# Kernel tuning notes

Measured on AMD Instinct MI355X. Metric: run time of the kernel, lower is better.

The kernel has to match this reference:

```python
import jax, jax.numpy as jnp
from jax import lax
import numpy as np

E, D, I, T, K = 32, 1024, 512, 4096, 8

def setup_inputs() -> dict:
    key = jax.random.key(0)
    k1, k2, k3, k4, k5 = jax.random.split(key, 5)
    hidden_states = jax.random.normal(k1, (T, D), dtype=jnp.float32)
    top_k_indices = jax.random.randint(k2, (T, K), 0, E, dtype=jnp.int64)
    w = jax.random.uniform(k3, (T, K), dtype=jnp.float32)
    top_k_weights = w / jnp.sum(w, axis=-1, keepdims=True)  # normalised routing weights
    gate_up_proj = jax.random.normal(k4, (E, 2 * I, D), dtype=jnp.float32) * 0.05
    down_proj = jax.random.normal(k5, (E, D, I), dtype=jnp.float32) * 0.05
    return {
        'hidden_states': hidden_states,
        'top_k_indices': top_k_indices,
        'top_k_weights': top_k_weights,
        'gate_up_proj': gate_up_proj,
        'down_proj': down_proj,
    }


def _moe(hidden_states, top_k_indices, top_k_weights, gate_up_proj, down_proj):
    num_experts = gate_up_proj.shape[0]
    # combine[t, e] = sum over k-slots routed to expert e of top_k_weights[t, k].
    # Duplicate expert ids in a token's top-k sum their weights, matching the
    # torch loop which index_add's each (k, tok) pair separately (outputs identical).
    onehot = jax.nn.one_hot(top_k_indices, num_experts, dtype=hidden_states.dtype)  # [T,K,E]
    combine = jnp.einsum('tke,tk->te', onehot, top_k_weights)  # [T,E]

    def body(acc, ew):
        W_gu, W_d, c = ew  # [2I,D], [D,I], [T]
        gu = hidden_states @ W_gu.T  # [T,2I]
        gate, up = jnp.split(gu, 2, axis=-1)
        h = jax.nn.silu(gate) * up  # SwiGLU
        y = h @ W_d.T  # [T,D]
        return acc + c[:, None] * y, None

    out, _ = lax.scan(body, jnp.zeros_like(hidden_states),
                      (gate_up_proj, down_proj, combine.T))
    return out


def reference(hidden_states, top_k_indices, top_k_weights, gate_up_proj, down_proj):
    return _moe(hidden_states, top_k_indices, top_k_weights, gate_up_proj, down_proj)
```

## Files before the change

kernel.cpp:

```cpp
#include <hip/hip_runtime.h>
#include <hip/hip_bf16.h>

#define E_   32
#define D_   1024
#define I_   512
#define T_   4096
#define KTOP 8
#define TK   (T_*KTOP)

#define BM   128
#define BKK  32
#define MAXT (TK/BM + E_)

#define TILES_OFF 1024
#define TOK_OFF   8192
#define WT_OFF    139264
#define H_OFF     524288

typedef __attribute__((ext_vector_type(8))) short short8v;
typedef __attribute__((ext_vector_type(4))) float f32x4;

__device__ inline unsigned short f2bf(float x) {
    union { float f; unsigned u; } v; v.f = x;
    return (unsigned short)((v.u + 0x7fff + ((v.u >> 16) & 1)) >> 16);
}
__device__ inline short8v pack8(float4 a, float4 b) {
    short8v r;
    r[0]=(short)f2bf(a.x); r[1]=(short)f2bf(a.y); r[2]=(short)f2bf(a.z); r[3]=(short)f2bf(a.w);
    r[4]=(short)f2bf(b.x); r[5]=(short)f2bf(b.y); r[6]=(short)f2bf(b.z); r[7]=(short)f2bf(b.w);
    return r;
}


__global__ void detect_idx64_kernel(const int* __restrict__ idx32, int* w) {
    if (threadIdx.x == 0 && blockIdx.x == 0) {
        int all0 = 1;
        for (int i = 0; i < 256; ++i)
            if (idx32[2*i + 1] != 0) { all0 = 0; break; }
        w[0] = all0;
    }
}

__global__ void count_kernel(const int* __restrict__ idx32, int* w) {
    int i = blockIdx.x * blockDim.x + threadIdx.x;
    if (i >= TK) return;
    int e = w[0] ? idx32[2*i] : idx32[i];
    atomicAdd(&w[32 + e], 1);
}

__global__ void scan_kernel(int* w) {
    if (threadIdx.x != 0 || blockIdx.x != 0) return;
    int off = 0;
    for (int e = 0; e < E_; ++e) { w[96 + e] = off; off += w[32 + e]; }
    w[96 + E_] = off;
    int2* tiles = (int2*)((char*)w + TILES_OFF);
    int nt = 0;
    for (int e = 0; e < E_; ++e)
        for (int rs = w[96 + e]; rs < w[96 + e + 1]; rs += BM)
            tiles[nt++] = make_int2(e, rs);
    w[129] = nt;
}

__global__ void scatter_kernel(const int* __restrict__ idx32,
                               const float* __restrict__ wts, int* w) {
    int i = blockIdx.x * blockDim.x + threadIdx.x;
    if (i >= TK) return;
    int e = w[0] ? idx32[2*i] : idx32[i];
    int p = atomicAdd(&w[64 + e], 1);
    int pos = w[96 + e] + p;
    ((int*)  ((char*)w + TOK_OFF))[pos] = i / KTOP;
    ((float*)((char*)w + WT_OFF))[pos]  = wts[i];
}

__global__ __launch_bounds__(256) void gemm1_mfma(
    const float* __restrict__ hidden, const float* __restrict__ gup,
    const int* __restrict__ w, unsigned short* __restrict__ H)
{
    if ((int)blockIdx.y >= w[129]) return;
    int2 tl = ((const int2*)((const char*)w + TILES_OFF))[blockIdx.y];
    const int e = tl.x, rs = tl.y;
    const int rows = min(w[96 + e + 1] - rs, BM);
    const int* tok = (const int*)((const char*)w + TOK_OFF);

    __shared__ short As[BM * BKK];
    __shared__ short Bs[BM * BKK];
    __shared__ int tokS[BM];

    const int tid = threadIdx.x;
    if (tid < BM) tokS[tid] = tok[rs + min(tid, rows - 1)];
    __syncthreads();

    const int n0 = blockIdx.x * 64;
    const float* gb = gup + (size_t)e * (2 * I_) * D_;

    const int crow = tid >> 2, ckg = tid & 3;
    const float* aptr0 = hidden + (size_t)tokS[crow]      * D_ + ckg * 8;
    const float* aptr1 = hidden + (size_t)tokS[crow + 64] * D_ + ckg * 8;
    const float* bptr0 = gb + (size_t)(n0 + crow)      * D_ + ckg * 8;
    const float* bptr1 = gb + (size_t)(I_ + n0 + crow) * D_ + ckg * 8;
    short8v* wA0 = (short8v*)&As[crow * BKK + ckg * 8];
    short8v* wA1 = (short8v*)&As[(crow + 64) * BKK + ckg * 8];
    short8v* wB0 = (short8v*)&Bs[crow * BKK + ckg * 8];
    short8v* wB1 = (short8v*)&Bs[(crow + 64) * BKK + ckg * 8];

    const int wid = tid >> 6, lane = tid & 63;
    const int l16 = lane & 15, lk = (lane >> 4) * 8;
    const int aoff = (wid * 32 + l16) * BKK + lk;
    const int boff = l16 * BKK + lk;

    f32x4 acc[2][8];
#pragma unroll
    for (int i = 0; i < 2; ++i)
#pragma unroll
        for (int j = 0; j < 8; ++j) acc[i][j] = (f32x4){0.f, 0.f, 0.f, 0.f};

    float4 ra0a, ra0b, ra1a, ra1b, rb0a, rb0b, rb1a, rb1b;
#define LOADREGS1(K0) { \
    ra0a = *(const float4*)(aptr0 + (K0)); ra0b = *(const float4*)(aptr0 + (K0) + 4); \
    ra1a = *(const float4*)(aptr1 + (K0)); ra1b = *(const float4*)(aptr1 + (K0) + 4); \
    rb0a = *(const float4*)(bptr0 + (K0)); rb0b = *(const float4*)(bptr0 + (K0) + 4); \
    rb1a = *(const float4*)(bptr1 + (K0)); rb1b = *(const float4*)(bptr1 + (K0) + 4); }

    LOADREGS1(0);
    for (int k0 = 0; k0 < D_; k0 += BKK) {
        __syncthreads();
        *wA0 = pack8(ra0a, ra0b);
        *wA1 = pack8(ra1a, ra1b);
        *wB0 = pack8(rb0a, rb0b);
        *wB1 = pack8(rb1a, rb1b);
        __syncthreads();
        if (k0 + BKK < D_) LOADREGS1(k0 + BKK);
        short8v a0 = *(const short8v*)&As[aoff];
        short8v a1 = *(const short8v*)&As[aoff + 16 * BKK];
#pragma unroll
        for (int j = 0; j < 8; ++j) {
            short8v b = *(const short8v*)&Bs[boff + j * 16 * BKK];
            acc[0][j] = __builtin_amdgcn_mfma_f32_16x16x32_bf16(a0, b, acc[0][j], 0, 0, 0);
            acc[1][j] = __builtin_amdgcn_mfma_f32_16x16x32_bf16(a1, b, acc[1][j], 0, 0, 0);
        }
    }

    const int r0 = (lane >> 4) * 4;
#pragma unroll
    for (int mr = 0; mr < 2; ++mr)
#pragma unroll
        for (int j = 0; j < 4; ++j)
#pragma unroll
            for (int r = 0; r < 4; ++r) {
                int m = wid * 32 + mr * 16 + r0 + r;
                if (m < rows) {
                    float g = acc[mr][j][r], u = acc[mr][j + 4][r];
                    float s = g / (1.f + __expf(-g));
                    H[(size_t)(rs + m) * I_ + n0 + j * 16 + l16] = f2bf(s * u);
                }
            }
}

__global__ __launch_bounds__(256) void gemm2_mfma(
    const unsigned short* __restrict__ H, const float* __restrict__ down,
    const int* __restrict__ w, float* __restrict__ out)
{
    if ((int)blockIdx.y >= w[129]) return;
    int2 tl = ((const int2*)((const char*)w + TILES_OFF))[blockIdx.y];
    const int e = tl.x, rs = tl.y;
    const int rows = min(w[96 + e + 1] - rs, BM);
    const int*   tok = (const int*)  ((const char*)w + TOK_OFF);
    const float* wts = (const float*)((const char*)w + WT_OFF);

    __shared__ short As[BM * BKK];
    __shared__ short Bs[BM * BKK];
    __shared__ int   tokS[BM];
    __shared__ float wtS[BM];

    const int tid = threadIdx.x;
    if (tid < BM) {
        tokS[tid] = tok[rs + min(tid, rows - 1)];
        wtS[tid]  = (tid < rows) ? wts[rs + tid] : 0.f;
    }
    __syncthreads();

    const int n0 = blockIdx.x * 128;
    const float* db = down + (size_t)e * D_ * I_;

    const int crow = tid >> 2, ckg = tid & 3;
    const short* ha0 = (const short*)H + (size_t)min(rs + crow,      TK - 1) * I_ + ckg * 8;
    const short* ha1 = (const short*)H + (size_t)min(rs + crow + 64, TK - 1) * I_ + ckg * 8;
    const float* bptr0 = db + (size_t)(n0 + crow)      * I_ + ckg * 8;
    const float* bptr1 = db + (size_t)(n0 + crow + 64) * I_ + ckg * 8;
    short8v* wA0 = (short8v*)&As[crow * BKK + ckg * 8];
    short8v* wA1 = (short8v*)&As[(crow + 64) * BKK + ckg * 8];
    short8v* wB0 = (short8v*)&Bs[crow * BKK + ckg * 8];
    short8v* wB1 = (short8v*)&Bs[(crow + 64) * BKK + ckg * 8];

    const int wid = tid >> 6, lane = tid & 63;
    const int l16 = lane & 15, lk = (lane >> 4) * 8;
    const int aoff = (wid * 32 + l16) * BKK + lk;
    const int boff = l16 * BKK + lk;

    f32x4 acc[2][8];
#pragma unroll
    for (int i = 0; i < 2; ++i)
#pragma unroll
        for (int j = 0; j < 8; ++j) acc[i][j] = (f32x4){0.f, 0.f, 0.f, 0.f};

    short8v raa, rab;
    float4 rb0a, rb0b, rb1a, rb1b;
#define LOADREGS2(K0) { \
    raa = *(const short8v*)(ha0 + (K0)); rab = *(const short8v*)(ha1 + (K0)); \
    rb0a = *(const float4*)(bptr0 + (K0)); rb0b = *(const float4*)(bptr0 + (K0) + 4); \
    rb1a = *(const float4*)(bptr1 + (K0)); rb1b = *(const float4*)(bptr1 + (K0) + 4); }

    LOADREGS2(0);
    for (int k0 = 0; k0 < I_; k0 += BKK) {
        __syncthreads();
        *wA0 = raa;
        *wA1 = rab;
        *wB0 = pack8(rb0a, rb0b);
        *wB1 = pack8(rb1a, rb1b);
        __syncthreads();
        if (k0 + BKK < I_) LOADREGS2(k0 + BKK);
        short8v a0 = *(const short8v*)&As[aoff];
        short8v a1 = *(const short8v*)&As[aoff + 16 * BKK];
#pragma unroll
        for (int j = 0; j < 8; ++j) {
            short8v b = *(const short8v*)&Bs[boff + j * 16 * BKK];
            acc[0][j] = __builtin_amdgcn_mfma_f32_16x16x32_bf16(a0, b, acc[0][j], 0, 0, 0);
            acc[1][j] = __builtin_amdgcn_mfma_f32_16x16x32_bf16(a1, b, acc[1][j], 0, 0, 0);
        }
    }

    const int r0 = (lane >> 4) * 4;
#pragma unroll
    for (int mr = 0; mr < 2; ++mr)
#pragma unroll
        for (int j = 0; j < 8; ++j)
#pragma unroll
            for (int r = 0; r < 4; ++r) {
                int m = wid * 32 + mr * 16 + r0 + r;
                if (m < rows)
                    atomicAdd(&out[(size_t)tokS[m] * D_ + n0 + j * 16 + l16],
                              wtS[m] * acc[mr][j][r]);
            }
}


extern "C" void kernel_launch(void* const* d_in, const int* in_sizes, int n_in,
                              void* d_out, int out_size, void* d_ws, size_t ws_size,
                              hipStream_t stream)
{
    const float* hidden = (const float*)d_in[0];
    const int*   idx    = (const int*)  d_in[1];
    const float* wts    = (const float*)d_in[2];
    const float* gup    = (const float*)d_in[3];
    const float* down   = (const float*)d_in[4];
    float* out = (float*)d_out;
    int*   w   = (int*)d_ws;

    hipMemsetAsync(d_ws, 0, 8192, stream);
    hipMemsetAsync(d_out, 0, (size_t)T_ * D_ * sizeof(float), stream);

    detect_idx64_kernel<<<1, 64, 0, stream>>>(idx, w);
    count_kernel<<<(TK + 255) / 256, 256, 0, stream>>>(idx, w);
    scan_kernel<<<1, 32, 0, stream>>>(w);
    scatter_kernel<<<(TK + 255) / 256, 256, 0, stream>>>(idx, wts, w);

    unsigned short* H = (unsigned short*)((char*)d_ws + H_OFF);
    dim3 g1(I_ / 64, MAXT), g2(D_ / 128, MAXT);
    gemm1_mfma<<<g1, 256, 0, stream>>>(hidden, gup, w, H);
    gemm2_mfma<<<g2, 256, 0, stream>>>(H, down, w, out);
}
```

Before: 733.0 us.

## Pad LDS tiles, parallelize scan and index detection, use library bf16 conversion

Pads the shared-memory A/B tiles from 32 to 40 shorts per row so the MFMA operand reads from LDS hit fewer bank conflicts. It also replaces the single-thread serial scan and tile-list construction with a wave-level shuffle prefix sum, and turns the int64-index detection loop into a parallel wave vote. The hand-written float-to-bf16 rounding is swapped for the HIP intrinsic. Together these target LDS conflict stalls in both GEMMs and serial latency in the small setup kernels, at the cost of more shared memory per block.

```diff
diff --git a/kernel.cpp b/kernel.cpp
--- a/kernel.cpp
+++ b/kernel.cpp
@@ -10,6 +10,7 @@
 
 #define BM   128
 #define BKK  32
+#define PAD  40
 #define MAXT (TK/BM + E_)
 
 #define TILES_OFF 1024
@@ -21,8 +22,8 @@
 typedef __attribute__((ext_vector_type(4))) float f32x4;
 
 __device__ inline unsigned short f2bf(float x) {
-    union { float f; unsigned u; } v; v.f = x;
-    return (unsigned short)((v.u + 0x7fff + ((v.u >> 16) & 1)) >> 16);
+    __hip_bfloat16 h = __float2bfloat16(x);
+    union { __hip_bfloat16 h; unsigned short u; } c; c.h = h; return c.u;
 }
 __device__ inline short8v pack8(float4 a, float4 b) {
     short8v r;
@@ -33,12 +34,12 @@
 
 
 __global__ void detect_idx64_kernel(const int* __restrict__ idx32, int* w) {
-    if (threadIdx.x == 0 && blockIdx.x == 0) {
-        int all0 = 1;
-        for (int i = 0; i < 256; ++i)
-            if (idx32[2*i + 1] != 0) { all0 = 0; break; }
-        w[0] = all0;
-    }
+    const int lane = threadIdx.x;
+    int bad = 0;
+#pragma unroll
+    for (int j = 0; j < 4; ++j) bad |= idx32[2 * (lane + 64 * j) + 1];
+    int allz = __all(bad == 0);
+    if (lane == 0) w[0] = allz ? 1 : 0;
 }
 
 __global__ void count_kernel(const int* __restrict__ idx32, int* w) {
@@ -49,16 +50,30 @@
 }
 
 __global__ void scan_kernel(int* w) {
-    if (threadIdx.x != 0 || blockIdx.x != 0) return;
-    int off = 0;
-    for (int e = 0; e < E_; ++e) { w[96 + e] = off; off += w[32 + e]; }
-    w[96 + E_] = off;
+    const int lane = threadIdx.x;
+    int cnt = (lane < E_) ? w[32 + lane] : 0;
+    int x = cnt;
+#pragma unroll
+    for (int d = 1; d < 32; d <<= 1) {
+        int v = __shfl_up(x, d, 64);
+        if (lane >= d) x += v;
+    }
+    int excl = x - cnt;
+    if (lane < E_) w[96 + lane] = excl;
+    if (lane == E_ - 1) w[96 + E_] = x;
+
+    int nt_e = (lane < E_) ? (cnt + BM - 1) / BM : 0;
+    int y = nt_e;
+#pragma unroll
+    for (int d = 1; d < 32; d <<= 1) {
+        int v = __shfl_up(y, d, 64);
+        if (lane >= d) y += v;
+    }
+    int texcl = y - nt_e;
+    if (lane == E_ - 1) w[129] = y;
     int2* tiles = (int2*)((char*)w + TILES_OFF);
-    int nt = 0;
-    for (int e = 0; e < E_; ++e)
-        for (int rs = w[96 + e]; rs < w[96 + e + 1]; rs += BM)
-            tiles[nt++] = make_int2(e, rs);
-    w[129] = nt;
+    for (int i = 0; i < nt_e; ++i)
+        tiles[texcl + i] = make_int2(lane, excl + i * BM);
 }
 
 __global__ void scatter_kernel(const int* __restrict__ idx32,
@@ -82,8 +97,8 @@
     const int rows = min(w[96 + e + 1] - rs, BM);
     const int* tok = (const int*)((const char*)w + TOK_OFF);
 
-    __shared__ short As[BM * BKK];
-    __shared__ short Bs[BM * BKK];
+    __shared__ short As[BM * PAD];
+    __shared__ short Bs[BM * PAD];
     __shared__ int tokS[BM];
 
     const int tid = threadIdx.x;
@@ -98,15 +113,15 @@
     const float* aptr1 = hidden + (size_t)tokS[crow + 64] * D_ + ckg * 8;
     const float* bptr0 = gb + (size_t)(n0 + crow)      * D_ + ckg * 8;
     const float* bptr1 = gb + (size_t)(I_ + n0 + crow) * D_ + ckg * 8;
-    short8v* wA0 = (short8v*)&As[crow * BKK + ckg * 8];
-    short8v* wA1 = (short8v*)&As[(crow + 64) * BKK + ckg * 8];
-    short8v* wB0 = (short8v*)&Bs[crow * BKK + ckg * 8];
-    short8v* wB1 = (short8v*)&Bs[(crow + 64) * BKK + ckg * 8];
+    short8v* wA0 = (short8v*)&As[crow * PAD + ckg * 8];
+    short8v* wA1 = (short8v*)&As[(crow + 64) * PAD + ckg * 8];
+    short8v* wB0 = (short8v*)&Bs[crow * PAD + ckg * 8];
+    short8v* wB1 = (short8v*)&Bs[(crow + 64) * PAD + ckg * 8];
 
     const int wid = tid >> 6, lane = tid & 63;
     const int l16 = lane & 15, lk = (lane >> 4) * 8;
-    const int aoff = (wid * 32 + l16) * BKK + lk;
-    const int boff = l16 * BKK + lk;
+    const int aoff = (wid * 32 + l16) * PAD + lk;
+    const int boff = l16 * PAD + lk;
 
     f32x4 acc[2][8];
 #pragma unroll
@@ -131,10 +146,10 @@
         __syncthreads();
         if (k0 + BKK < D_) LOADREGS1(k0 + BKK);
         short8v a0 = *(const short8v*)&As[aoff];
-        short8v a1 = *(const short8v*)&As[aoff + 16 * BKK];
+        short8v a1 = *(const short8v*)&As[aoff + 16 * PAD];
 #pragma unroll
         for (int j = 0; j < 8; ++j) {
-            short8v b = *(const short8v*)&Bs[boff + j * 16 * BKK];
+            short8v b = *(const short8v*)&Bs[boff + j * 16 * PAD];
             acc[0][j] = __builtin_amdgcn_mfma_f32_16x16x32_bf16(a0, b, acc[0][j], 0, 0, 0);
             acc[1][j] = __builtin_amdgcn_mfma_f32_16x16x32_bf16(a1, b, acc[1][j], 0, 0, 0);
         }
@@ -167,8 +182,8 @@
     const int*   tok = (const int*)  ((const char*)w + TOK_OFF);
     const float* wts = (const float*)((const char*)w + WT_OFF);
 
-    __shared__ short As[BM * BKK];
-    __shared__ short Bs[BM * BKK];
+    __shared__ short As[BM * PAD];
+    __shared__ short Bs[BM * PAD];
     __shared__ int   tokS[BM];
     __shared__ float wtS[BM];
 
@@ -187,15 +202,15 @@
     const short* ha1 = (const short*)H + (size_t)min(rs + crow + 64, TK - 1) * I_ + ckg * 8;
     const float* bptr0 = db + (size_t)(n0 + crow)      * I_ + ckg * 8;
     const float* bptr1 = db + (size_t)(n0 + crow + 64) * I_ + ckg * 8;
-    short8v* wA0 = (short8v*)&As[crow * BKK + ckg * 8];
-    short8v* wA1 = (short8v*)&As[(crow + 64) * BKK + ckg * 8];
-    short8v* wB0 = (short8v*)&Bs[crow * BKK + ckg * 8];
-    short8v* wB1 = (short8v*)&Bs[(crow + 64) * BKK + ckg * 8];
+    short8v* wA0 = (short8v*)&As[crow * PAD + ckg * 8];
+    short8v* wA1 = (short8v*)&As[(crow + 64) * PAD + ckg * 8];
+    short8v* wB0 = (short8v*)&Bs[crow * PAD + ckg * 8];
+    short8v* wB1 = (short8v*)&Bs[(crow + 64) * PAD + ckg * 8];
 
     const int wid = tid >> 6, lane = tid & 63;
     const int l16 = lane & 15, lk = (lane >> 4) * 8;
-    const int aoff = (wid * 32 + l16) * BKK + lk;
-    const int boff = l16 * BKK + lk;
+    const int aoff = (wid * 32 + l16) * PAD + lk;
+    const int boff = l16 * PAD + lk;
 
     f32x4 acc[2][8];
 #pragma unroll
@@ -220,10 +235,10 @@
         __syncthreads();
         if (k0 + BKK < I_) LOADREGS2(k0 + BKK);
         short8v a0 = *(const short8v*)&As[aoff];
-        short8v a1 = *(const short8v*)&As[aoff + 16 * BKK];
+        short8v a1 = *(const short8v*)&As[aoff + 16 * PAD];
 #pragma unroll
         for (int j = 0; j < 8; ++j) {
-            short8v b = *(const short8v*)&Bs[boff + j * 16 * BKK];
+            short8v b = *(const short8v*)&Bs[boff + j * 16 * PAD];
             acc[0][j] = __builtin_amdgcn_mfma_f32_16x16x32_bf16(a0, b, acc[0][j], 0, 0, 0);
             acc[1][j] = __builtin_amdgcn_mfma_f32_16x16x32_bf16(a1, b, acc[1][j], 0, 0, 0);
         }
@@ -261,7 +276,7 @@
 
     detect_idx64_kernel<<<1, 64, 0, stream>>>(idx, w);
     count_kernel<<<(TK + 255) / 256, 256, 0, stream>>>(idx, w);
-    scan_kernel<<<1, 32, 0, stream>>>(w);
+    scan_kernel<<<1, 64, 0, stream>>>(w);
     scatter_kernel<<<(TK + 255) / 256, 256, 0, stream>>>(idx, wts, w);
 
     unsigned short* H = (unsigned short*)((char*)d_ws + H_OFF);
```

Result: faster. 687.4 us (-6.2%).
